# Performance work log

Measured on AMD Instinct MI355X. Metric: run time of the kernel, lower is better.

## Reference

```python
import jax, jax.numpy as jnp
import numpy as np

B, S, D, NH = 1024, 128, 512, 8
DH = D // NH  # head dim = 64


def setup_inputs() -> dict:
    key = jax.random.key(0)
    ks = jax.random.split(key, 9)
    scale = 1.0 / np.sqrt(D)
    return {
        "x_non": jax.random.normal(ks[0], (B, D), jnp.float32),
        "x_seq": jax.random.normal(ks[1], (B, S, D), jnp.float32),
        "mask": jax.random.randint(ks[2], (B, NH, S), 0, 2, jnp.int32),
        "Wq": jax.random.normal(ks[3], (D, D), jnp.float32) * scale,
        "bq": jax.random.normal(ks[4], (D,), jnp.float32) * scale,
        "Wk": jax.random.normal(ks[5], (D, D), jnp.float32) * scale,
        "bk": jax.random.normal(ks[6], (D,), jnp.float32) * scale,
        "Wv": jax.random.normal(ks[7], (D, D), jnp.float32) * scale,
        "bv": jax.random.normal(ks[8], (D,), jnp.float32) * scale,
    }


def reference(x_non, x_seq, mask, Wq, bq, Wk, bk, Wv, bv):
    batch, seq_len, dim = x_seq.shape
    nhead = NH
    dh = dim // nhead
    # Linear projections (torch Linear: y = x @ W.T + b)
    q = (x_non @ Wq.T + bq).reshape(batch, nhead, dh)           # (b, n, d)
    k = (x_seq @ Wk.T + bk).reshape(batch, seq_len, nhead, dh)  # (b, s, n, d)
    v = (x_seq @ Wv.T + bv).reshape(batch, seq_len, nhead, dh)
    qk = jnp.einsum("bnd,bsnd->bns", q, k)
    # NOTE: source uses `//` (floor division) by sqrt(d_head) -- reproduced faithfully
    qk = jnp.floor(qk / jnp.sqrt(jnp.asarray(dh, qk.dtype)))
    qk = jnp.where(mask == 0, jnp.asarray(-1e9, qk.dtype), qk)
    attn = jax.nn.softmax(qk, axis=-1)                           # (b, n, s)
    z = jnp.einsum("bns,bsnd->bnd", attn, v).reshape(batch, dim)
    return z
```

## Files before the change

### kernel.cpp

```cpp
#include <hip/hip_runtime.h>

#define SS  128
#define DD  512
#define NHH 8
#define DHH 64

typedef float  f4 __attribute__((ext_vector_type(4)));
typedef double d2 __attribute__((ext_vector_type(2)));

__global__ __launch_bounds__(256) void qproj_kernel(
    const float* __restrict__ x_non, const float* __restrict__ Wq,
    const float* __restrict__ bq, double* __restrict__ qws)
{
    const int tid = threadIdx.x;
    const int bt  = blockIdx.x & 31;
    const int ot  = blockIdx.x >> 5;
    const int r   = tid >> 4, c = tid & 15;

    __shared__ __attribute__((aligned(16))) float Xs[32][68];
    __shared__ __attribute__((aligned(16))) float Ws[64][68];

    double acc[2][4];
    #pragma unroll
    for (int i = 0; i < 2; ++i)
        #pragma unroll
        for (int j = 0; j < 4; ++j) acc[i][j] = 0.0;

    for (int kc = 0; kc < 8; ++kc) {
        __syncthreads();
        #pragma unroll
        for (int p = 0; p < 2; ++p) {
            int s = tid + 256 * p, rr = s >> 4, cc = (s & 15) * 4;
            *(f4*)&Xs[rr][cc] = *(const f4*)(x_non + (size_t)(bt * 32 + rr) * DD + kc * 64 + cc);
        }
        #pragma unroll
        for (int p = 0; p < 4; ++p) {
            int s = tid + 256 * p, rr = s >> 4, cc = (s & 15) * 4;
            *(f4*)&Ws[rr][cc] = *(const f4*)(Wq + (size_t)(ot * 64 + rr) * DD + kc * 64 + cc);
        }
        __syncthreads();
        #pragma unroll 4
        for (int kk = 0; kk < 64; ++kk) {
            double a0 = (double)Xs[r][kk];
            double a1 = (double)Xs[r + 16][kk];
            #pragma unroll
            for (int j = 0; j < 4; ++j) {
                double bb = (double)Ws[c + 16 * j][kk];
                acc[0][j] = fma(a0, bb, acc[0][j]);
                acc[1][j] = fma(a1, bb, acc[1][j]);
            }
        }
    }
    #pragma unroll
    for (int i = 0; i < 2; ++i)
        #pragma unroll
        for (int j = 0; j < 4; ++j) {
            int o = ot * 64 + c + 16 * j;
            qws[(size_t)(bt * 32 + r + 16 * i) * DD + o] = acc[i][j] + (double)bq[o];
        }
}

__global__ __launch_bounds__(256) void core_kernel(
    const double* __restrict__ qws, const float* __restrict__ x_seq,
    const int* __restrict__ mask, const float* __restrict__ Wk,
    const float* __restrict__ bk, float* __restrict__ uws)
{
    const int tid = threadIdx.x;
    const int b   = blockIdx.x;
    const float* Xb = x_seq + (size_t)b * (SS * DD);

    __shared__ __attribute__((aligned(16))) union {
        double T[8][512];
        double P[4][8][128];
    } sh;
    __shared__ __attribute__((aligned(16))) union {
        double qd[512];
        float  attn[8][128];
    } sh2;
    __shared__ double qbks[8];
    __shared__ float  lsums[8];

    sh2.qd[tid]       = qws[(size_t)b * DD + tid];
    sh2.qd[tid + 256] = qws[(size_t)b * DD + tid + 256];
    __syncthreads();

    if (tid < 64) {
        const int h = tid >> 3, part = tid & 7;
        double s = 0.0;
        #pragma unroll
        for (int ii = 0; ii < 8; ++ii) {
            int d = part * 8 + ii;
            s = fma(sh2.qd[h * DHH + d], (double)bk[h * DHH + d], s);
        }
        s += __shfl_xor(s, 1);
        s += __shfl_xor(s, 2);
        s += __shfl_xor(s, 4);
        if (part == 0) qbks[h] = s;
    }

    {
        const int kg = tid & 127, dh = tid >> 7;
        const int k4 = kg * 4;
        for (int hg = 0; hg < 2; ++hg) {
            double tacc[4][4];
            #pragma unroll
            for (int h4 = 0; h4 < 4; ++h4) {
                const int h = hg * 4 + h4;
                const float* wp = Wk + ((size_t)(h * DHH + dh * 32)) * DD + k4;
                double t0 = 0, t1 = 0, t2 = 0, t3 = 0;
                for (int d = 0; d < 32; ++d) {
                    f4 wv = *(const f4*)(wp + (size_t)d * DD);
                    double qv = sh2.qd[h * DHH + dh * 32 + d];
                    t0 = fma((double)wv[0], qv, t0);
                    t1 = fma((double)wv[1], qv, t1);
                    t2 = fma((double)wv[2], qv, t2);
                    t3 = fma((double)wv[3], qv, t3);
                }
                tacc[h4][0] = t0; tacc[h4][1] = t1; tacc[h4][2] = t2; tacc[h4][3] = t3;
            }
            if (dh == 1) {
                #pragma unroll
                for (int h4 = 0; h4 < 4; ++h4)
                    #pragma unroll
                    for (int e = 0; e < 4; ++e)
                        sh.T[hg * 4 + h4][k4 + e] = tacc[h4][e];
            }
            __syncthreads();
            if (dh == 0) {
                #pragma unroll
                for (int h4 = 0; h4 < 4; ++h4)
                    #pragma unroll
                    for (int e = 0; e < 4; ++e)
                        sh.T[hg * 4 + h4][k4 + e] += tacc[h4][e];
            }
            __syncthreads();
        }
    }

    const int qw = tid >> 6, l = tid & 63;
    double acc0[8], acc1[8];
    #pragma unroll
    for (int h = 0; h < 8; ++h) { acc0[h] = 0.0; acc1[h] = 0.0; }
    {
        const int k0 = qw * 128;
        const float* xa = Xb + (size_t)l * DD + k0;
        const float* xc = xa + (size_t)64 * DD;
        for (int j = 0; j < 128; j += 4) {
            f4 xva = *(const f4*)(xa + j);
            f4 xvc = *(const f4*)(xc + j);
            #pragma unroll
            for (int h = 0; h < 8; ++h) {
                d2 t01 = *(const d2*)&sh.T[h][k0 + j];
                d2 t23 = *(const d2*)&sh.T[h][k0 + j + 2];
                acc0[h] = fma((double)xva[0], t01[0], acc0[h]);
                acc1[h] = fma((double)xvc[0], t01[0], acc1[h]);
                acc0[h] = fma((double)xva[1], t01[1], acc0[h]);
                acc1[h] = fma((double)xvc[1], t01[1], acc1[h]);
                acc0[h] = fma((double)xva[2], t23[0], acc0[h]);
                acc1[h] = fma((double)xvc[2], t23[0], acc1[h]);
                acc0[h] = fma((double)xva[3], t23[1], acc0[h]);
                acc1[h] = fma((double)xvc[3], t23[1], acc1[h]);
            }
        }
    }
    __syncthreads();
    #pragma unroll
    for (int h = 0; h < 8; ++h) {
        sh.P[qw][h][l]      = acc0[h];
        sh.P[qw][h][l + 64] = acc1[h];
    }
    __syncthreads();

    #pragma unroll
    for (int p = 0; p < 4; ++p) {
        int slot = tid + 256 * p;
        int h = slot >> 7, s2 = slot & 127;
        double tot = sh.P[0][h][s2] + sh.P[1][h][s2]
                   + sh.P[2][h][s2] + sh.P[3][h][s2] + qbks[h];
        double sc = floor(tot * 0.125);
        if (mask[(size_t)b * (NHH * SS) + slot] == 0) sc = -1e9;
        sh2.attn[h][s2] = (float)sc;
    }
    __syncthreads();

    {
        const int h = tid >> 5, i = tid & 31;
        float v[4], mx = -3e38f;
        #pragma unroll
        for (int jj = 0; jj < 4; ++jj) { v[jj] = sh2.attn[h][i + 32 * jj]; mx = fmaxf(mx, v[jj]); }
        #pragma unroll
        for (int off = 1; off < 32; off <<= 1) mx = fmaxf(mx, __shfl_xor(mx, off, 32));
        float sum = 0.f;
        #pragma unroll
        for (int jj = 0; jj < 4; ++jj) { v[jj] = expf(v[jj] - mx); sum += v[jj]; }
        #pragma unroll
        for (int off = 1; off < 32; off <<= 1) sum += __shfl_xor(sum, off, 32);
        #pragma unroll
        for (int jj = 0; jj < 4; ++jj) sh2.attn[h][i + 32 * jj] = v[jj];
        if (i == 0) lsums[h] = sum;
    }
    __syncthreads();

    {
        float a1[8], a2[8];
        #pragma unroll
        for (int h = 0; h < 8; ++h) { a1[h] = 0.f; a2[h] = 0.f; }
        for (int s2 = 0; s2 < SS; s2 += 4) {
            f4 av[8];
            #pragma unroll
            for (int h = 0; h < 8; ++h) av[h] = *(const f4*)&sh2.attn[h][s2];
            #pragma unroll
            for (int e = 0; e < 4; ++e) {
                float x1 = Xb[(size_t)(s2 + e) * DD + tid];
                float x2 = Xb[(size_t)(s2 + e) * DD + tid + 256];
                #pragma unroll
                for (int h = 0; h < 8; ++h) {
                    a1[h] = fmaf(av[h][e], x1, a1[h]);
                    a2[h] = fmaf(av[h][e], x2, a2[h]);
                }
            }
        }
        #pragma unroll
        for (int h = 0; h < 8; ++h) {
            float inv = 1.0f / lsums[h];
            uws[((size_t)b * NHH + h) * DD + tid]       = a1[h] * inv;
            uws[((size_t)b * NHH + h) * DD + tid + 256] = a2[h] * inv;
        }
    }
}

__global__ __launch_bounds__(256) void zout_kernel(
    const float* __restrict__ uws, const float* __restrict__ Wv,
    const float* __restrict__ bv, float* __restrict__ out)
{
    const int tid = threadIdx.x;
    const int bt  = blockIdx.x & 31;
    const int ot  = blockIdx.x >> 5;
    const int r   = tid >> 4, c = tid & 15;

    __shared__ __attribute__((aligned(16))) float Us[32][68];
    __shared__ __attribute__((aligned(16))) float Ws[64][68];

    float acc[2][4];
    #pragma unroll
    for (int i = 0; i < 2; ++i)
        #pragma unroll
        for (int j = 0; j < 4; ++j) acc[i][j] = 0.f;

    for (int kc = 0; kc < 8; ++kc) {
        __syncthreads();
        #pragma unroll
        for (int p = 0; p < 2; ++p) {
            int s = tid + 256 * p, rr = s >> 4, cc = (s & 15) * 4;
            *(f4*)&Us[rr][cc] =
                *(const f4*)(uws + ((size_t)(bt * 32 + rr) * NHH + ot) * DD + kc * 64 + cc);
        }
        #pragma unroll
        for (int p = 0; p < 4; ++p) {
            int s = tid + 256 * p, rr = s >> 4, cc = (s & 15) * 4;
            *(f4*)&Ws[rr][cc] = *(const f4*)(Wv + (size_t)(ot * 64 + rr) * DD + kc * 64 + cc);
        }
        __syncthreads();
        #pragma unroll 4
        for (int kk = 0; kk < 64; ++kk) {
            float a0 = Us[r][kk];
            float a1 = Us[r + 16][kk];
            #pragma unroll
            for (int j = 0; j < 4; ++j) {
                float bb = Ws[c + 16 * j][kk];
                acc[0][j] = fmaf(a0, bb, acc[0][j]);
                acc[1][j] = fmaf(a1, bb, acc[1][j]);
            }
        }
    }
    #pragma unroll
    for (int i = 0; i < 2; ++i)
        #pragma unroll
        for (int j = 0; j < 4; ++j) {
            int o = ot * 64 + c + 16 * j;
            out[(size_t)(bt * 32 + r + 16 * i) * DD + o] = acc[i][j] + bv[o];
        }
}

extern "C" void kernel_launch(void* const* d_in, const int* in_sizes, int n_in,
                              void* d_out, int out_size, void* d_ws, size_t ws_size,
                              hipStream_t stream) {
    const float* x_non = (const float*)d_in[0];
    const float* x_seq = (const float*)d_in[1];
    const int*   mask  = (const int*)d_in[2];
    const float* Wq    = (const float*)d_in[3];
    const float* bq    = (const float*)d_in[4];
    const float* Wk    = (const float*)d_in[5];
    const float* bk    = (const float*)d_in[6];
    const float* Wv    = (const float*)d_in[7];
    const float* bv    = (const float*)d_in[8];
    float*       out   = (float*)d_out;

    double* qws = (double*)d_ws;
    float*  uws = (float*)((char*)d_ws + (size_t)1024 * DD * 8);

    qproj_kernel<<<256, 256, 0, stream>>>(x_non, Wq, bq, qws);
    core_kernel<<<1024, 256, 0, stream>>>(qws, x_seq, mask, Wk, bk, uws);
    zout_kernel<<<256, 256, 0, stream>>>(uws, Wv, bv, out);
}
```

Measured before the change: 529.5 us.

## Precompute per-batch q·Wk projection in a separate kernel and smaller GEMM tiles

Moves the per-batch T = q_h·Wk_h product (the query folded into the key weights) out of the core kernel into a new tproj kernel with a batched GEMM across 2048 blocks. It also writes q·bk per head to the workspace, so the core kernel only streams the precomputed T into shared memory and does the x_seq dot products. The q-projection and output GEMMs get smaller tiles and twice as many blocks for better occupancy. The cost is an extra launch, a 32MB double-precision workspace written and then read back, and a fallback path used when the workspace is too small.

```diff
diff --git a/kernel.cpp b/kernel.cpp
--- a/kernel.cpp
+++ b/kernel.cpp
@@ -13,25 +13,20 @@
     const float* __restrict__ bq, double* __restrict__ qws)
 {
     const int tid = threadIdx.x;
-    const int bt  = blockIdx.x & 31;
-    const int ot  = blockIdx.x >> 5;
-    const int r   = tid >> 4, c = tid & 15;
-
-    __shared__ __attribute__((aligned(16))) float Xs[32][68];
+    const int ot  = blockIdx.x & 7;
+    const int bt  = blockIdx.x >> 3;
+    const int r0  = tid >> 4, c0 = tid & 15;
+
+    __shared__ __attribute__((aligned(16))) float Xs[16][68];
     __shared__ __attribute__((aligned(16))) float Ws[64][68];
 
-    double acc[2][4];
-    #pragma unroll
-    for (int i = 0; i < 2; ++i)
-        #pragma unroll
-        for (int j = 0; j < 4; ++j) acc[i][j] = 0.0;
+    double acc[4] = {0.0, 0.0, 0.0, 0.0};
 
     for (int kc = 0; kc < 8; ++kc) {
         __syncthreads();
-        #pragma unroll
-        for (int p = 0; p < 2; ++p) {
-            int s = tid + 256 * p, rr = s >> 4, cc = (s & 15) * 4;
-            *(f4*)&Xs[rr][cc] = *(const f4*)(x_non + (size_t)(bt * 32 + rr) * DD + kc * 64 + cc);
+        {
+            int rr = tid >> 4, cc = (tid & 15) * 4;
+            *(f4*)&Xs[rr][cc] = *(const f4*)(x_non + (size_t)(bt * 16 + rr) * DD + kc * 64 + cc);
         }
         #pragma unroll
         for (int p = 0; p < 4; ++p) {
@@ -41,26 +36,197 @@
         __syncthreads();
         #pragma unroll 4
         for (int kk = 0; kk < 64; ++kk) {
-            double a0 = (double)Xs[r][kk];
-            double a1 = (double)Xs[r + 16][kk];
-            #pragma unroll
-            for (int j = 0; j < 4; ++j) {
-                double bb = (double)Ws[c + 16 * j][kk];
-                acc[0][j] = fma(a0, bb, acc[0][j]);
-                acc[1][j] = fma(a1, bb, acc[1][j]);
-            }
-        }
-    }
+            double x = (double)Xs[r0][kk];
+            #pragma unroll
+            for (int j = 0; j < 4; ++j)
+                acc[j] = fma(x, (double)Ws[c0 + 16 * j][kk], acc[j]);
+        }
+    }
+    #pragma unroll
+    for (int j = 0; j < 4; ++j) {
+        int o = ot * 64 + c0 + 16 * j;
+        qws[(size_t)(bt * 16 + r0) * DD + o] = acc[j] + (double)bq[o];
+    }
+}
+
+__global__ __launch_bounds__(256) void tproj_kernel(
+    const double* __restrict__ qws, const float* __restrict__ Wk,
+    const float* __restrict__ bk, double* __restrict__ tws,
+    double* __restrict__ qbkws)
+{
+    const int tid = threadIdx.x;
+    const int h   = blockIdx.x & 7;
+    const int bt  = (blockIdx.x >> 3) & 31;
+    const int kt  = blockIdx.x >> 8;
+    const int r0  = tid >> 4, c0 = tid & 15;
+
+    __shared__ __attribute__((aligned(16))) double qs[32][66];
+    __shared__ __attribute__((aligned(16))) float  Wks[64][68];
+
+    #pragma unroll
+    for (int i = 0; i < 8; ++i) {
+        int flat = tid + 256 * i;
+        int r = flat >> 6, d = flat & 63;
+        qs[r][d] = qws[(size_t)(bt * 32 + r) * DD + h * DHH + d];
+    }
+    #pragma unroll
+    for (int i = 0; i < 4; ++i) {
+        int flat = tid + 256 * i;
+        int d = flat >> 4, c4 = (flat & 15) * 4;
+        *(f4*)&Wks[d][c4] = *(const f4*)(Wk + (size_t)(h * DHH + d) * DD + kt * 64 + c4);
+    }
+    __syncthreads();
+
+    double acc[2][4];
     #pragma unroll
     for (int i = 0; i < 2; ++i)
         #pragma unroll
+        for (int j = 0; j < 4; ++j) acc[i][j] = 0.0;
+
+    #pragma unroll 4
+    for (int d = 0; d < 64; ++d) {
+        double q0 = qs[r0][d];
+        double q1 = qs[r0 + 16][d];
+        #pragma unroll
         for (int j = 0; j < 4; ++j) {
-            int o = ot * 64 + c + 16 * j;
-            qws[(size_t)(bt * 32 + r + 16 * i) * DD + o] = acc[i][j] + (double)bq[o];
-        }
+            double w = (double)Wks[d][c0 + 16 * j];
+            acc[0][j] = fma(q0, w, acc[0][j]);
+            acc[1][j] = fma(q1, w, acc[1][j]);
+        }
+    }
+    #pragma unroll
+    for (int i = 0; i < 2; ++i)
+        #pragma unroll
+        for (int j = 0; j < 4; ++j) {
+            int b = bt * 32 + r0 + 16 * i;
+            int k = kt * 64 + c0 + 16 * j;
+            tws[(size_t)b * (NHH * DD) + h * DD + k] = acc[i][j];
+        }
+
+    if (kt == 0 && tid < 32) {
+        double s = 0.0;
+        for (int d = 0; d < DHH; ++d)
+            s = fma(qs[tid][d], (double)bk[h * DHH + d], s);
+        qbkws[(size_t)(bt * 32 + tid) * NHH + h] = s;
+    }
 }
 
 __global__ __launch_bounds__(256) void core_kernel(
+    const double* __restrict__ tws, const double* __restrict__ qbkws,
+    const float* __restrict__ x_seq, const int* __restrict__ mask,
+    float* __restrict__ uws)
+{
+    const int tid = threadIdx.x;
+    const int b   = blockIdx.x;
+    const float* Xb = x_seq + (size_t)b * (SS * DD);
+
+    __shared__ __attribute__((aligned(16))) union {
+        double Tl[NHH * DD];
+        double P[4][8][128];
+    } sh;
+    __shared__ __attribute__((aligned(16))) float attn[8][128];
+    __shared__ double qbks[8];
+    __shared__ float  lsums[8];
+
+    #pragma unroll
+    for (int i = 0; i < 16; ++i)
+        sh.Tl[tid + 256 * i] = tws[(size_t)b * (NHH * DD) + tid + 256 * i];
+    if (tid < 8) qbks[tid] = qbkws[(size_t)b * NHH + tid];
+    __syncthreads();
+
+    const int qw = tid >> 6, l = tid & 63;
+    double acc0[8], acc1[8];
+    #pragma unroll
+    for (int h = 0; h < 8; ++h) { acc0[h] = 0.0; acc1[h] = 0.0; }
+    {
+        const int k0 = qw * 128;
+        const float* xa = Xb + (size_t)l * DD + k0;
+        const float* xc = xa + (size_t)64 * DD;
+        for (int j = 0; j < 128; j += 4) {
+            f4 xva = *(const f4*)(xa + j);
+            f4 xvc = *(const f4*)(xc + j);
+            #pragma unroll
+            for (int h = 0; h < 8; ++h) {
+                d2 t01 = *(const d2*)&sh.Tl[h * DD + k0 + j];
+                d2 t23 = *(const d2*)&sh.Tl[h * DD + k0 + j + 2];
+                acc0[h] = fma((double)xva[0], t01[0], acc0[h]);
+                acc1[h] = fma((double)xvc[0], t01[0], acc1[h]);
+                acc0[h] = fma((double)xva[1], t01[1], acc0[h]);
+                acc1[h] = fma((double)xvc[1], t01[1], acc1[h]);
+                acc0[h] = fma((double)xva[2], t23[0], acc0[h]);
+                acc1[h] = fma((double)xvc[2], t23[0], acc1[h]);
+                acc0[h] = fma((double)xva[3], t23[1], acc0[h]);
+                acc1[h] = fma((double)xvc[3], t23[1], acc1[h]);
+            }
+        }
+    }
+    __syncthreads();
+    #pragma unroll
+    for (int h = 0; h < 8; ++h) {
+        sh.P[qw][h][l]      = acc0[h];
+        sh.P[qw][h][l + 64] = acc1[h];
+    }
+    __syncthreads();
+
+    #pragma unroll
+    for (int p = 0; p < 4; ++p) {
+        int slot = tid + 256 * p;
+        int h = slot >> 7, s2 = slot & 127;
+        double tot = sh.P[0][h][s2] + sh.P[1][h][s2]
+                   + sh.P[2][h][s2] + sh.P[3][h][s2] + qbks[h];
+        double sc = floor(tot * 0.125);
+        if (mask[(size_t)b * (NHH * SS) + slot] == 0) sc = -1e9;
+        attn[h][s2] = (float)sc;
+    }
+    __syncthreads();
+
+    {
+        const int h = tid >> 5, i = tid & 31;
+        float v[4], mx = -3e38f;
+        #pragma unroll
+        for (int jj = 0; jj < 4; ++jj) { v[jj] = attn[h][i + 32 * jj]; mx = fmaxf(mx, v[jj]); }
+        #pragma unroll
+        for (int off = 1; off < 32; off <<= 1) mx = fmaxf(mx, __shfl_xor(mx, off, 32));
+        float sum = 0.f;
+        #pragma unroll
+        for (int jj = 0; jj < 4; ++jj) { v[jj] = expf(v[jj] - mx); sum += v[jj]; }
+        #pragma unroll
+        for (int off = 1; off < 32; off <<= 1) sum += __shfl_xor(sum, off, 32);
+        #pragma unroll
+        for (int jj = 0; jj < 4; ++jj) attn[h][i + 32 * jj] = v[jj];
+        if (i == 0) lsums[h] = sum;
+    }
+    __syncthreads();
+
+    {
+        float a1[8], a2[8];
+        #pragma unroll
+        for (int h = 0; h < 8; ++h) { a1[h] = 0.f; a2[h] = 0.f; }
+        for (int s2 = 0; s2 < SS; s2 += 4) {
+            f4 av[8];
+            #pragma unroll
+            for (int h = 0; h < 8; ++h) av[h] = *(const f4*)&attn[h][s2];
+            #pragma unroll
+            for (int e = 0; e < 4; ++e) {
+                float x1 = Xb[(size_t)(s2 + e) * DD + tid];
+                float x2 = Xb[(size_t)(s2 + e) * DD + tid + 256];
+                #pragma unroll
+                for (int h = 0; h < 8; ++h) {
+                    a1[h] = fmaf(av[h][e], x1, a1[h]);
+                    a2[h] = fmaf(av[h][e], x2, a2[h]);
+                }
+            }
+        }
+        #pragma unroll
+        for (int h = 0; h < 8; ++h) {
+            float inv = 1.0f / lsums[h];
+            uws[((size_t)b * NHH + h) * DD + tid]       = a1[h] * inv;
+            uws[((size_t)b * NHH + h) * DD + tid + 256] = a2[h] * inv;
+        }
+    }
+}
+
+__global__ __launch_bounds__(256) void core_fallback_kernel(
     const double* __restrict__ qws, const float* __restrict__ x_seq,
     const int* __restrict__ mask, const float* __restrict__ Wk,
     const float* __restrict__ bk, float* __restrict__ uws)
@@ -234,18 +400,15 @@
     const float* __restrict__ bv, float* __restrict__ out)
 {
     const int tid = threadIdx.x;
-    const int bt  = blockIdx.x & 31;
-    const int ot  = blockIdx.x >> 5;
-    const int r   = tid >> 4, c = tid & 15;
+    const int ot  = blockIdx.x & 15;
+    const int bt  = blockIdx.x >> 4;
+    const int h   = ot >> 1;
+    const int r0  = tid >> 4, c0 = tid & 15;
 
     __shared__ __attribute__((aligned(16))) float Us[32][68];
-    __shared__ __attribute__((aligned(16))) float Ws[64][68];
-
-    float acc[2][4];
-    #pragma unroll
-    for (int i = 0; i < 2; ++i)
-        #pragma unroll
-        for (int j = 0; j < 4; ++j) acc[i][j] = 0.f;
+    __shared__ __attribute__((aligned(16))) float Ws[32][68];
+
+    float acc[2][2] = {{0.f, 0.f}, {0.f, 0.f}};
 
     for (int kc = 0; kc < 8; ++kc) {
         __syncthreads();
@@ -253,32 +416,29 @@
         for (int p = 0; p < 2; ++p) {
             int s = tid + 256 * p, rr = s >> 4, cc = (s & 15) * 4;
             *(f4*)&Us[rr][cc] =
-                *(const f4*)(uws + ((size_t)(bt * 32 + rr) * NHH + ot) * DD + kc * 64 + cc);
-        }
-        #pragma unroll
-        for (int p = 0; p < 4; ++p) {
-            int s = tid + 256 * p, rr = s >> 4, cc = (s & 15) * 4;
-            *(f4*)&Ws[rr][cc] = *(const f4*)(Wv + (size_t)(ot * 64 + rr) * DD + kc * 64 + cc);
+                *(const f4*)(uws + ((size_t)(bt * 32 + rr) * NHH + h) * DD + kc * 64 + cc);
+            *(f4*)&Ws[rr][cc] =
+                *(const f4*)(Wv + (size_t)(ot * 32 + rr) * DD + kc * 64 + cc);
         }
         __syncthreads();
         #pragma unroll 4
         for (int kk = 0; kk < 64; ++kk) {
-            float a0 = Us[r][kk];
-            float a1 = Us[r + 16][kk];
-            #pragma unroll
-            for (int j = 0; j < 4; ++j) {
-                float bb = Ws[c + 16 * j][kk];
-                acc[0][j] = fmaf(a0, bb, acc[0][j]);
-                acc[1][j] = fmaf(a1, bb, acc[1][j]);
-            }
+            float u0 = Us[r0][kk];
+            float u1 = Us[r0 + 16][kk];
+            float w0 = Ws[c0][kk];
+            float w1 = Ws[c0 + 16][kk];
+            acc[0][0] = fmaf(u0, w0, acc[0][0]);
+            acc[0][1] = fmaf(u0, w1, acc[0][1]);
+            acc[1][0] = fmaf(u1, w0, acc[1][0]);
+            acc[1][1] = fmaf(u1, w1, acc[1][1]);
         }
     }
     #pragma unroll
     for (int i = 0; i < 2; ++i)
         #pragma unroll
-        for (int j = 0; j < 4; ++j) {
-            int o = ot * 64 + c + 16 * j;
-            out[(size_t)(bt * 32 + r + 16 * i) * DD + o] = acc[i][j] + bv[o];
+        for (int j = 0; j < 2; ++j) {
+            int o = ot * 32 + c0 + 16 * j;
+            out[(size_t)(bt * 32 + r0 + 16 * i) * DD + o] = acc[i][j] + bv[o];
         }
 }
 
@@ -296,10 +456,26 @@
     const float* bv    = (const float*)d_in[8];
     float*       out   = (float*)d_out;
 
-    double* qws = (double*)d_ws;
-    float*  uws = (float*)((char*)d_ws + (size_t)1024 * DD * 8);
-
-    qproj_kernel<<<256, 256, 0, stream>>>(x_non, Wq, bq, qws);
-    core_kernel<<<1024, 256, 0, stream>>>(qws, x_seq, mask, Wk, bk, uws);
-    zout_kernel<<<256, 256, 0, stream>>>(uws, Wv, bv, out);
-}
+    const size_t SZ_A   = (size_t)16 * 1024 * 1024;
+    const size_t SZ_T   = (size_t)32 * 1024 * 1024;
+    const size_t SZ_QBK = (size_t)1024 * NHH * 8;
+    const size_t NEED   = SZ_A + SZ_T + SZ_QBK;
+
+    if (ws_size >= NEED) {
+        double* qws   = (double*)d_ws;
+        float*  uws   = (float*)d_ws;
+        double* tws   = (double*)((char*)d_ws + SZ_A);
+        double* qbkws = (double*)((char*)d_ws + SZ_A + SZ_T);
+
+        qproj_kernel<<<512, 256, 0, stream>>>(x_non, Wq, bq, qws);
+        tproj_kernel<<<2048, 256, 0, stream>>>(qws, Wk, bk, tws, qbkws);
+        core_kernel<<<1024, 256, 0, stream>>>(tws, qbkws, x_seq, mask, uws);
+        zout_kernel<<<512, 256, 0, stream>>>(uws, Wv, bv, out);
+    } else {
+        double* qws = (double*)d_ws;
+        float*  uws = (float*)((char*)d_ws + (size_t)1024 * DD * 8);
+        qproj_kernel<<<512, 256, 0, stream>>>(x_non, Wq, bq, qws);
+        core_fallback_kernel<<<1024, 256, 0, stream>>>(qws, x_seq, mask, Wk, bk, uws);
+        zout_kernel<<<512, 256, 0, stream>>>(uws, Wv, bv, out);
+    }
+}
```

Measured after the change: 683.0 us. +29.0%, slower.
